# Performance work log

Measured on AMD Instinct MI355X. Metric: run time of the kernel, lower is better.

## Reference

```python
import jax, jax.numpy as jnp
import numpy as np

N = 50000      # n_nodes == ninput
E = 800000     # edges
NHID = 96
N_INTER = 6
EPS = 1e-12


def _l2norm(x):
    # F.normalize(x, p=2, dim=1) with eps=1e-12
    n = jnp.linalg.norm(x, axis=1, keepdims=True)
    return x / jnp.maximum(n, EPS)


def _sage(x, src, dst, Wl, bl, Wr, n):
    # PyG SAGEConv (mean aggr): lin_l(mean_{j in N(i)} x_j) + lin_r(x_i)
    agg = jax.ops.segment_sum(x[src], dst, num_segments=n)          # [N, nhid]
    deg = jax.ops.segment_sum(jnp.ones((src.shape[0],), x.dtype), dst, num_segments=n)
    agg = agg / jnp.maximum(deg, 1.0)[:, None]
    return agg @ Wl + bl + x @ Wr


def _mlp(x, W1, b1, W2, b2, W3, b3):
    # GNN-Bet score MLP (eval mode, dropout p=0): nhid -> 2*nhid -> 2*nhid -> 1
    h = jax.nn.relu(x @ W1 + b1)
    h = jax.nn.relu(h @ W2 + b2)
    return h @ W3 + b3


def setup_inputs() -> dict:
    key = jax.random.key(0)
    ks = jax.random.split(key, 16)
    s = 0.05
    inp = {
        'edge_index1': jax.random.randint(ks[0], (2, E), 0, N, dtype=jnp.int32),
        'edge_vals1': jax.random.uniform(ks[1], (E,), dtype=jnp.float32),
        'edge_index2': jax.random.randint(ks[2], (2, E), 0, N, dtype=jnp.int32),
        # GNN_Layer_Init: weight [ninput=N, nhid], bias [nhid]
        'gc1_W': jax.random.normal(ks[3], (N, NHID), dtype=jnp.float32) * s,
        'gc1_b': jnp.zeros((NHID,), jnp.float32),
        # 7 SAGEConv layers (6 intermediate + gc_last), stacked
        'sage_Wl': jax.random.normal(ks[4], (7, NHID, NHID), dtype=jnp.float32) * s,
        'sage_bl': jnp.zeros((7, NHID), jnp.float32),
        'sage_Wr': jax.random.normal(ks[5], (7, NHID, NHID), dtype=jnp.float32) * s,
        # score MLP
        'mlp_W1': jax.random.normal(ks[6], (NHID, 2 * NHID), dtype=jnp.float32) * s,
        'mlp_b1': jnp.zeros((2 * NHID,), jnp.float32),
        'mlp_W2': jax.random.normal(ks[7], (2 * NHID, 2 * NHID), dtype=jnp.float32) * s,
        'mlp_b2': jnp.zeros((2 * NHID,), jnp.float32),
        'mlp_W3': jax.random.normal(ks[8], (2 * NHID, 1), dtype=jnp.float32) * s,
        'mlp_b3': jnp.zeros((1,), jnp.float32),
    }
    return inp


def reference(edge_index1, edge_vals1, edge_index2, gc1_W, gc1_b,
              sage_Wl, sage_bl, sage_Wr,
              mlp_W1, mlp_b1, mlp_W2, mlp_b2, mlp_W3, mlp_b3):
    # gc1: spmm(adj1, W) -> out[i] = sum_j adj1[i,j] * W[j]
    dst1, src1 = edge_index1[0], edge_index1[1]
    h0 = jax.ops.segment_sum(gc1_W[src1] * edge_vals1[:, None], dst1, num_segments=N) + gc1_b
    x2_1 = _l2norm(jax.nn.relu(h0))

    src2, dst2 = edge_index2[0], edge_index2[1]

    # main trunk: 6 intermediate SAGE layers applied sequentially
    x = x2_1
    for i in range(N_INTER):
        x = _l2norm(jax.nn.relu(_sage(x, src2, dst2, sage_Wl[i], sage_bl[i], sage_Wr[i], N)))
    x_last = jax.nn.relu(_sage(x, src2, dst2, sage_Wl[N_INTER], sage_bl[N_INTER], sage_Wr[N_INTER], N))

    # scores: MLP on x2_1, on each intermediate layer applied once to x2_1, and on x_last
    score = _mlp(x2_1, mlp_W1, mlp_b1, mlp_W2, mlp_b2, mlp_W3, mlp_b3)
    for i in range(N_INTER):
        xi = _l2norm(jax.nn.relu(_sage(x2_1, src2, dst2, sage_Wl[i], sage_bl[i], sage_Wr[i], N)))
        score = score + _mlp(xi, mlp_W1, mlp_b1, mlp_W2, mlp_b2, mlp_W3, mlp_b3)
    score = score + _mlp(x_last, mlp_W1, mlp_b1, mlp_W2, mlp_b2, mlp_W3, mlp_b3)
    return score  # [N, 1]
```

## Files before the change

### kernel.cpp

```cpp
#include <hip/hip_runtime.h>

#define NH 96
#define NH2 192

typedef __attribute__((ext_vector_type(8))) short short8;
typedef __attribute__((ext_vector_type(4))) float f32x4;

__device__ __forceinline__ unsigned short f2b(float f) {
  unsigned u = __float_as_uint(f);
  unsigned r = (u + 0x7FFFu + ((u >> 16) & 1u)) >> 16;
  return (unsigned short)r;
}
__device__ __forceinline__ float blo(unsigned w) { return __uint_as_float(w << 16); }
__device__ __forceinline__ float bhi(unsigned w) { return __uint_as_float(w & 0xFFFF0000u); }
__device__ __forceinline__ float b2f(short v) { return __uint_as_float(((unsigned)(unsigned short)v) << 16); }

__device__ __forceinline__ unsigned cvt_pk(float lo, float hi) {
  unsigned r;
  asm("v_cvt_pk_bf16_f32 %0, %1, %2" : "=v"(r) : "v"(lo), "v"(hi));
  return r;
}

__device__ __forceinline__ short8 u4_to_s8(int a, int b, int c, int d) {
  union { int u[4]; short8 s; } x;
  x.u[0] = a; x.u[1] = b; x.u[2] = c; x.u[3] = d;
  return x.s;
}

#define MFMA(a, b, c) __builtin_amdgcn_mfma_f32_16x16x32_bf16((a), (b), (c), 0, 0, 0)
#define WFRAG(p, idx) (*(const short8*)((p) + ((idx) << 9) + (l << 3)))

__device__ __forceinline__ void stage(unsigned short* dst, const unsigned short* src, int nshorts,
                                      int tid, int nt) {
  const uint4* s = (const uint4*)src;
  uint4* d = (uint4*)dst;
  int nv = nshorts >> 3;
  for (int i = tid; i < nv; i += nt) d[i] = s[i];
}

__device__ __forceinline__ short8 xchg(unsigned p0lo, unsigned p0hi, unsigned p1lo, unsigned p1hi,
                                       int srcA, int srcB, int hi) {
  int a0 = __shfl((int)p0lo, srcA), a1 = __shfl((int)p0hi, srcA);
  int c0 = __shfl((int)p1lo, srcA), c1 = __shfl((int)p1hi, srcA);
  int b0 = __shfl((int)p0lo, srcB), b1 = __shfl((int)p0hi, srcB);
  int d0 = __shfl((int)p1lo, srcB), d1 = __shfl((int)p1hi, srcB);
  return u4_to_s8(hi ? c0 : a0, hi ? c1 : a1, hi ? d0 : b0, hi ? d1 : b1);
}


__global__ void k_count(const int* __restrict__ dst1, const int* __restrict__ dst2,
                        int* __restrict__ cnt1, int* __restrict__ cnt2, int E, int psize) {
  int p = blockIdx.x & 7;
  int e = (blockIdx.x >> 3) * blockDim.x + threadIdx.x;
  if (e >= E) return;
  int lo = p * psize, hi = lo + psize;
  int d = dst1[e];
  if (d >= lo && d < hi) atomicAdd(&cnt1[d], 1);
  int dd = dst2[e];
  if (dd >= lo && dd < hi) atomicAdd(&cnt2[dd], 1);
}


__global__ __launch_bounds__(256) void k_scanA(const int* __restrict__ cnt1, const int* __restrict__ cnt2,
                                               int* __restrict__ bs, int n) {
  int seg = blockIdx.y;
  const int* cnt = seg ? cnt2 : cnt1;
  int t = threadIdx.x;
  int idx = blockIdx.x * 1024 + t * 4;
  int sum = 0;
  if (idx + 3 < n) {
    int4 v = *(const int4*)(cnt + idx);
    sum = v.x + v.y + v.z + v.w;
  } else {
    for (int j = 0; j < 4; ++j) if (idx + j < n) sum += cnt[idx + j];
  }
  __shared__ int s[256];
  s[t] = sum;
  __syncthreads();
  for (int off = 128; off > 0; off >>= 1) {
    if (t < off) s[t] += s[t + off];
    __syncthreads();
  }
  if (t == 0) bs[seg * 64 + blockIdx.x] = s[0];
}

__global__ __launch_bounds__(128) void k_scanB(int* __restrict__ bs, int* __restrict__ rp1,
                                               int* __restrict__ rp2, int nb, int n) {
  int w = threadIdx.x >> 6, l = threadIdx.x & 63;
  int v = (l < nb) ? bs[w * 64 + l] : 0;
  int incl = v;
  for (int off = 1; off < 64; off <<= 1) {
    int u = __shfl_up(incl, off);
    if (l >= off) incl += u;
  }
  if (l < nb) bs[w * 64 + l] = incl - v;
  if (l == 63) {
    int* rp = w ? rp2 : rp1;
    rp[n] = incl;
  }
}

__global__ __launch_bounds__(256) void k_scanC(const int* __restrict__ cnt1, const int* __restrict__ cnt2,
                                               const int* __restrict__ bs,
                                               int* __restrict__ rp1, int* __restrict__ cur1,
                                               int* __restrict__ rp2, int* __restrict__ cur2, int n) {
  int seg = blockIdx.y;
  const int* cnt = seg ? cnt2 : cnt1;
  int* rp = seg ? rp2 : rp1;
  int* cur = seg ? cur2 : cur1;
  int t = threadIdx.x;
  int idx = blockIdx.x * 1024 + t * 4;
  int v[4] = {0, 0, 0, 0};
  if (idx + 3 < n) {
    int4 q = *(const int4*)(cnt + idx);
    v[0] = q.x; v[1] = q.y; v[2] = q.z; v[3] = q.w;
  } else {
    for (int j = 0; j < 4; ++j) if (idx + j < n) v[j] = cnt[idx + j];
  }
  int tsum = v[0] + v[1] + v[2] + v[3];
  __shared__ int s[256];
  s[t] = tsum;
  __syncthreads();
  for (int off = 1; off < 256; off <<= 1) {
    int u = (t >= off) ? s[t - off] : 0;
    __syncthreads();
    s[t] += u;
    __syncthreads();
  }
  int run = (t == 0 ? 0 : s[t - 1]) + bs[seg * 64 + blockIdx.x];
  for (int j = 0; j < 4; ++j) {
    if (idx + j < n) {
      rp[idx + j] = run;
      cur[idx + j] = run;
      run += v[j];
    }
  }
}

__global__ __launch_bounds__(1024) void k_scan(const int* __restrict__ cnt, int* __restrict__ rp,
                                               int* __restrict__ cur, int n) {
  __shared__ int s[1024];
  int tid = threadIdx.x;
  int chunk = (n + 1023) >> 10;
  int beg = tid * chunk;
  int end = min(beg + chunk, n);
  int sum = 0;
  for (int i = beg; i < end; ++i) sum += cnt[i];
  s[tid] = sum;
  __syncthreads();
  for (int off = 1; off < 1024; off <<= 1) {
    int v = (tid >= off) ? s[tid - off] : 0;
    __syncthreads();
    s[tid] += v;
    __syncthreads();
  }
  int excl = (tid == 0) ? 0 : s[tid - 1];
  for (int i = beg; i < end; ++i) { rp[i] = excl; cur[i] = excl; excl += cnt[i]; }
  if (tid == 1023) rp[n] = s[1023];
}

__global__ void k_scatter(const int* __restrict__ d1, const int* __restrict__ s1, const float* __restrict__ v1,
                          int* __restrict__ cur1, int2* __restrict__ c1sv,
                          const int* __restrict__ s2, const int* __restrict__ d2,
                          int* __restrict__ cur2, int* __restrict__ c2s, int E, int psize) {
  int p = blockIdx.x & 7;
  int e = (blockIdx.x >> 3) * blockDim.x + threadIdx.x;
  if (e >= E) return;
  int lo = p * psize, hi = lo + psize;
  int d = d1[e];
  if (d >= lo && d < hi) {
    int pos = atomicAdd(&cur1[d], 1);
    c1sv[pos] = make_int2(s1[e], __float_as_int(v1[e]));
  }
  int dd = d2[e];
  if (dd >= lo && dd < hi) {
    int pos = atomicAdd(&cur2[dd], 1);
    c2s[pos] = s2[e];
  }
}


__global__ void k_prep(const float* __restrict__ Wl, const float* __restrict__ Wr,
                       const float* __restrict__ W1, const float* __restrict__ W2,
                       const float* __restrict__ gW,
                       unsigned short* __restrict__ Wlp, unsigned short* __restrict__ Wrp,
                       unsigned short* __restrict__ W1p, unsigned short* __restrict__ W2p,
                       unsigned short* __restrict__ gwb, int gtotal) {
  int t = blockIdx.x * blockDim.x + threadIdx.x;
  if (t < 129024) {
    bool isR = t >= 64512;
    int u = isR ? t - 64512 : t;
    int i = u / 9216, v = u % 9216;
    int tt = v / 1536, r = v % 1536;
    int kf = r / 512, w = r % 512, l = w >> 3, j = w & 7;
    int c = l & 15, g = l >> 4;
    int k = kf * 32 + g * 8 + j, nn = tt * 16 + c;
    float val = (isR ? Wr : Wl)[i * 9216 + k * 96 + nn];
    (isR ? Wrp : Wlp)[u] = f2b(val);
  } else if (t < 147456) {
    int u = t - 129024;
    int tt = u / 1536, r = u % 1536;
    int kf = r / 512, w = r % 512, l = w >> 3, j = w & 7;
    int c = l & 15, g = l >> 4;
    int k = kf * 32 + g * 8 + j, nn = tt * 16 + c;
    W1p[u] = f2b(W1[k * 192 + nn]);
  } else if (t < 184320) {
    int u = t - 147456;
    int tt = u / 3072, r = u % 3072;
    int kf = r / 512, w = r % 512, l = w >> 3, j = w & 7;
    int c = l & 15, g = l >> 4;
    int k = kf * 32 + g * 8 + j, nn = tt * 16 + c;
    W2p[u] = f2b(W2[k * 192 + nn]);
  } else {
    int i = (t - 184320) * 4;
    if (i + 3 < gtotal) {
      float4 v = *(const float4*)(gW + i);
      ushort4 o;
      o.x = f2b(v.x); o.y = f2b(v.y); o.z = f2b(v.z); o.w = f2b(v.w);
      *(ushort4*)(gwb + i) = o;
    }
  }
}


__global__ __launch_bounds__(256) void k_gc1(const int* __restrict__ rp, const int2* __restrict__ cv,
                                             const unsigned short* __restrict__ Wb,
                                             const float* __restrict__ b, unsigned short* __restrict__ out, int n) {
  int gw = (blockIdx.x * 256 + threadIdx.x) >> 6;
  int l = threadIdx.x & 63;
  if (gw >= n) return;
  int s = rp[gw], e = rp[gw + 1];
  bool act = l < 48;
  float a0 = 0.f, a1 = 0.f, b0 = 0.f, b1 = 0.f, c0 = 0.f, c1 = 0.f, d0 = 0.f, d1 = 0.f;
  int i = s;
  for (; i + 3 < e; i += 4) {
    int2 q0 = cv[i], q1 = cv[i + 1], q2 = cv[i + 2], q3 = cv[i + 3];
    if (act) {
      unsigned w0 = *(const unsigned*)(Wb + (size_t)q0.x * NH + 2 * l);
      unsigned w1 = *(const unsigned*)(Wb + (size_t)q1.x * NH + 2 * l);
      unsigned w2 = *(const unsigned*)(Wb + (size_t)q2.x * NH + 2 * l);
      unsigned w3 = *(const unsigned*)(Wb + (size_t)q3.x * NH + 2 * l);
      float v0 = __int_as_float(q0.y), v1 = __int_as_float(q1.y);
      float v2 = __int_as_float(q2.y), v3 = __int_as_float(q3.y);
      a0 = fmaf(v0, blo(w0), a0); a1 = fmaf(v0, bhi(w0), a1);
      b0 = fmaf(v1, blo(w1), b0); b1 = fmaf(v1, bhi(w1), b1);
      c0 = fmaf(v2, blo(w2), c0); c1 = fmaf(v2, bhi(w2), c1);
      d0 = fmaf(v3, blo(w3), d0); d1 = fmaf(v3, bhi(w3), d1);
    }
  }
  for (; i < e; ++i) {
    int2 q0 = cv[i];
    if (act) {
      unsigned w0 = *(const unsigned*)(Wb + (size_t)q0.x * NH + 2 * l);
      float v0 = __int_as_float(q0.y);
      a0 = fmaf(v0, blo(w0), a0); a1 = fmaf(v0, bhi(w0), a1);
    }
  }
  a0 += b0 + c0 + d0; a1 += b1 + c1 + d1;
  if (act) {
    a0 = fmaxf(a0 + b[2 * l], 0.f);
    a1 = fmaxf(a1 + b[2 * l + 1], 0.f);
  } else { a0 = a1 = 0.f; }
  float ss = a0 * a0 + a1 * a1;
#pragma unroll
  for (int o = 1; o < 64; o <<= 1) ss += __shfl_xor(ss, o);
  float sc = 1.f / fmaxf(sqrtf(ss), 1e-12f);
  if (act) {
    unsigned pk = ((unsigned)f2b(a1 * sc) << 16) | f2b(a0 * sc);
    ((unsigned*)out)[(size_t)gw * 48 + l] = pk;
  }
}


__global__ __launch_bounds__(256) void k_agg(const int* __restrict__ rp, const int* __restrict__ csrc,
                                             const unsigned short* __restrict__ X,
                                             unsigned short* __restrict__ out, int n) {
  int gw = (blockIdx.x * 256 + threadIdx.x) >> 6;
  int l = threadIdx.x & 63;
  if (gw >= n) return;
  int s = rp[gw], e = rp[gw + 1];
  bool act = l < 48;
  float a0 = 0.f, a1 = 0.f, b0 = 0.f, b1 = 0.f, c0 = 0.f, c1 = 0.f, d0 = 0.f, d1 = 0.f;
  int i = s;
  for (; i + 3 < e; i += 4) {
    int s0 = csrc[i], s1 = csrc[i + 1], s2 = csrc[i + 2], s3 = csrc[i + 3];
    if (act) {
      unsigned w0 = *(const unsigned*)(X + (size_t)s0 * NH + 2 * l);
      unsigned w1 = *(const unsigned*)(X + (size_t)s1 * NH + 2 * l);
      unsigned w2 = *(const unsigned*)(X + (size_t)s2 * NH + 2 * l);
      unsigned w3 = *(const unsigned*)(X + (size_t)s3 * NH + 2 * l);
      a0 += blo(w0); a1 += bhi(w0);
      b0 += blo(w1); b1 += bhi(w1);
      c0 += blo(w2); c1 += bhi(w2);
      d0 += blo(w3); d1 += bhi(w3);
    }
  }
  for (; i < e; ++i) {
    int s0 = csrc[i];
    if (act) {
      unsigned w0 = *(const unsigned*)(X + (size_t)s0 * NH + 2 * l);
      a0 += blo(w0); a1 += bhi(w0);
    }
  }
  a0 += b0 + c0 + d0; a1 += b1 + c1 + d1;
  float inv = 1.f / fmaxf((float)(e - s), 1.f);
  if (act) {
    unsigned pk = ((unsigned)f2b(a1 * inv) << 16) | f2b(a0 * inv);
    ((unsigned*)out)[(size_t)gw * 48 + l] = pk;
  }
}


template <int EPI>
__global__ __launch_bounds__(256) void k_sageagg(const int* __restrict__ rp, const int* __restrict__ csrc,
                                                 const unsigned short* __restrict__ X,
                                                 const unsigned short* __restrict__ Wlp,
                                                 const unsigned short* __restrict__ Wrp,
                                                 const float* __restrict__ bias,
                                                 unsigned short* __restrict__ Y, int n) {
  __shared__ __align__(16) unsigned short sw[18432];
  int tid = threadIdx.x;
  int l = tid & 63;
  int m0 = (blockIdx.x * 4 + (tid >> 6)) * 16;
  int c = l & 15, g = l >> 4;

  stage(sw, Wlp, 9216, tid, 256);
  stage(sw + 9216, Wrp, 9216, tid, 256);
  __syncthreads();

  int nd = min(m0 + c, n - 1);
  int s = rp[nd], e = rp[nd + 1];

  float aa[3][8], bb[3][8];
#pragma unroll
  for (int kf = 0; kf < 3; ++kf)
#pragma unroll
    for (int j = 0; j < 8; ++j) { aa[kf][j] = 0.f; bb[kf][j] = 0.f; }

  const unsigned short* Xg = X + g * 8;
  int i = s;
  for (; i + 1 < e; i += 2) {
    const unsigned short* xr0 = Xg + (size_t)csrc[i] * NH;
    const unsigned short* xr1 = Xg + (size_t)csrc[i + 1] * NH;
    short8 a0 = *(const short8*)(xr0);
    short8 a1 = *(const short8*)(xr0 + 32);
    short8 a2 = *(const short8*)(xr0 + 64);
    short8 b0 = *(const short8*)(xr1);
    short8 b1 = *(const short8*)(xr1 + 32);
    short8 b2 = *(const short8*)(xr1 + 64);
#pragma unroll
    for (int j = 0; j < 8; ++j) {
      aa[0][j] += b2f(a0[j]); aa[1][j] += b2f(a1[j]); aa[2][j] += b2f(a2[j]);
      bb[0][j] += b2f(b0[j]); bb[1][j] += b2f(b1[j]); bb[2][j] += b2f(b2[j]);
    }
  }
  if (i < e) {
    const unsigned short* xr0 = Xg + (size_t)csrc[i] * NH;
    short8 a0 = *(const short8*)(xr0);
    short8 a1 = *(const short8*)(xr0 + 32);
    short8 a2 = *(const short8*)(xr0 + 64);
#pragma unroll
    for (int j = 0; j < 8; ++j) {
      aa[0][j] += b2f(a0[j]); aa[1][j] += b2f(a1[j]); aa[2][j] += b2f(a2[j]);
    }
  }
  float inv = 1.f / fmaxf((float)(e - s), 1.f);
  short8 af[3];
#pragma unroll
  for (int kf = 0; kf < 3; ++kf)
#pragma unroll
    for (int j = 0; j < 8; ++j) af[kf][j] = (short)f2b((aa[kf][j] + bb[kf][j]) * inv);

  size_t aoff = (size_t)nd * NH + g * 8;
  short8 xf[3];
#pragma unroll
  for (int kf = 0; kf < 3; ++kf) xf[kf] = *(const short8*)(X + aoff + kf * 32);

  f32x4 acc[6];
#pragma unroll
  for (int t = 0; t < 6; ++t) acc[t] = (f32x4){0.f, 0.f, 0.f, 0.f};
#pragma unroll
  for (int kf = 0; kf < 3; ++kf) {
#pragma unroll
    for (int t = 0; t < 6; ++t) {
      short8 wlf = WFRAG(sw, t * 3 + kf);
      acc[t] = MFMA(wlf, af[kf], acc[t]);
    }
#pragma unroll
    for (int t = 0; t < 6; ++t) {
      short8 wrf = WFRAG(sw + 9216, t * 3 + kf);
      acc[t] = MFMA(wrf, xf[kf], acc[t]);
    }
  }

  float v[6][4];
  float ss = 0.f;
#pragma unroll
  for (int t = 0; t < 6; ++t) {
    float4 bv = *(const float4*)(bias + t * 16 + g * 4);
#pragma unroll
    for (int r = 0; r < 4; ++r) {
      float x = fmaxf(acc[t][r] + ((const float*)&bv)[r], 0.f);
      v[t][r] = x;
      ss = fmaf(x, x, ss);
    }
  }
  if (EPI == 0) {
    ss += __shfl_xor(ss, 16);
    ss += __shfl_xor(ss, 32);
    float sc = 1.f / fmaxf(sqrtf(ss), 1e-12f);
#pragma unroll
    for (int t = 0; t < 6; ++t)
#pragma unroll
      for (int r = 0; r < 4; ++r) v[t][r] *= sc;
  }
  if (m0 + c < n) {
    unsigned short* yr = Y + (size_t)(m0 + c) * NH;
#pragma unroll
    for (int t = 0; t < 6; ++t)
      *(uint2*)(yr + t * 16 + g * 4) = make_uint2(cvt_pk(v[t][0], v[t][1]), cvt_pk(v[t][2], v[t][3]));
  }
}


__global__ __launch_bounds__(256) void k_mlp(const unsigned short* __restrict__ X,
                                             const unsigned short* __restrict__ W1p, const float* __restrict__ b1,
                                             const unsigned short* __restrict__ W2p, const float* __restrict__ b2,
                                             const float* __restrict__ W3, const float* __restrict__ b3,
                                             float* __restrict__ score, int n) {
  __shared__ __align__(16) unsigned short sw[18432];
  int tid = threadIdx.x;
  int l = tid & 63;
  int m0 = (blockIdx.x * 4 + (tid >> 6)) * 32;
  int c = l & 15, g = l >> 4;
  int srcA = c + ((g & 1) << 5), srcB = srcA + 16, hi = g >> 1;
  int rA = min(m0 + c, n - 1), rB = min(m0 + 16 + c, n - 1);

  stage(sw, W1p, 18432, tid, 256);

  short8 xf[2][3];
#pragma unroll
  for (int kf = 0; kf < 3; ++kf) {
    xf[0][kf] = *(const short8*)(X + (size_t)rA * NH + kf * 32 + g * 8);
    xf[1][kf] = *(const short8*)(X + (size_t)rB * NH + kf * 32 + g * 8);
  }
  __syncthreads();

  unsigned pk1[2][12][2];
#pragma unroll
  for (int t = 0; t < 12; ++t) {
    f32x4 a0 = (f32x4){0.f, 0.f, 0.f, 0.f};
    f32x4 a1 = (f32x4){0.f, 0.f, 0.f, 0.f};
#pragma unroll
    for (int kf = 0; kf < 3; ++kf) {
      short8 wf = WFRAG(sw, t * 3 + kf);
      a0 = MFMA(wf, xf[0][kf], a0);
      a1 = MFMA(wf, xf[1][kf], a1);
    }
    float4 bv = *(const float4*)(b1 + t * 16 + g * 4);
    pk1[0][t][0] = cvt_pk(fmaxf(a0[0] + bv.x, 0.f), fmaxf(a0[1] + bv.y, 0.f));
    pk1[0][t][1] = cvt_pk(fmaxf(a0[2] + bv.z, 0.f), fmaxf(a0[3] + bv.w, 0.f));
    pk1[1][t][0] = cvt_pk(fmaxf(a1[0] + bv.x, 0.f), fmaxf(a1[1] + bv.y, 0.f));
    pk1[1][t][1] = cvt_pk(fmaxf(a1[2] + bv.z, 0.f), fmaxf(a1[3] + bv.w, 0.f));
  }

  short8 af2[2][6];
#pragma unroll
  for (int kf = 0; kf < 6; ++kf) {
    af2[0][kf] = xchg(pk1[0][2 * kf][0], pk1[0][2 * kf][1], pk1[0][2 * kf + 1][0], pk1[0][2 * kf + 1][1], srcA, srcB, hi);
    af2[1][kf] = xchg(pk1[1][2 * kf][0], pk1[1][2 * kf][1], pk1[1][2 * kf + 1][0], pk1[1][2 * kf + 1][1], srcA, srcB, hi);
  }

  float sv0 = 0.f, sv1 = 0.f;
#pragma unroll
  for (int h = 0; h < 2; ++h) {
    __syncthreads();
    stage(sw, W2p + h * 18432, 18432, tid, 256);
    __syncthreads();
#pragma unroll
    for (int tt = 0; tt < 6; ++tt) {
      int t = h * 6 + tt;
      f32x4 a0 = (f32x4){0.f, 0.f, 0.f, 0.f};
      f32x4 a1 = (f32x4){0.f, 0.f, 0.f, 0.f};
#pragma unroll
      for (int kf = 0; kf < 6; ++kf) {
        short8 wf = WFRAG(sw, tt * 6 + kf);
        a0 = MFMA(wf, af2[0][kf], a0);
        a1 = MFMA(wf, af2[1][kf], a1);
      }
      float4 bv = *(const float4*)(b2 + t * 16 + g * 4);
      float4 wv3 = *(const float4*)(W3 + t * 16 + g * 4);
#pragma unroll
      for (int r = 0; r < 4; ++r) {
        sv0 = fmaf(fmaxf(a0[r] + ((const float*)&bv)[r], 0.f), ((const float*)&wv3)[r], sv0);
        sv1 = fmaf(fmaxf(a1[r] + ((const float*)&bv)[r], 0.f), ((const float*)&wv3)[r], sv1);
      }
    }
  }
  sv0 += __shfl_xor(sv0, 16); sv0 += __shfl_xor(sv0, 32);
  sv1 += __shfl_xor(sv1, 16); sv1 += __shfl_xor(sv1, 32);
  if (g == 0) {
    float b3v = b3[0];
    if (m0 + c < n) score[m0 + c] += sv0 + b3v;
    if (m0 + 16 + c < n) score[m0 + 16 + c] += sv1 + b3v;
  }
}


__global__ __launch_bounds__(512) void k_branch(const unsigned short* __restrict__ Ag,
                                                const unsigned short* __restrict__ X21,
                                                const unsigned short* __restrict__ Wlp,
                                                const unsigned short* __restrict__ Wrp,
                                                const float* __restrict__ sbl,
                                                const unsigned short* __restrict__ W1p, const float* __restrict__ b1,
                                                const unsigned short* __restrict__ W2p, const float* __restrict__ b2,
                                                const float* __restrict__ W3, const float* __restrict__ b3,
                                                unsigned short* __restrict__ Xb, float* __restrict__ score,
                                                int n, int nblk) {
  __shared__ __align__(16) unsigned short sw[18432];
  int bb = blockIdx.x / nblk;
  int blk = blockIdx.x - bb * nblk;
  int tid = threadIdx.x;
  int l = tid & 63;
  int m0 = (blk * 8 + (tid >> 6)) * 32;
  int c = l & 15, g = l >> 4;
  int srcA = c + ((g & 1) << 5), srcB = srcA + 16, hi = g >> 1;
  int rA = min(m0 + c, n - 1), rB = min(m0 + 16 + c, n - 1);
  size_t aoffA = (size_t)rA * NH + g * 8, aoffB = (size_t)rB * NH + g * 8;

  short8 af1[2][3];

  if (bb < 6) {
    const float* bl = sbl + (size_t)bb * NH;
    stage(sw, Wlp + (size_t)bb * 9216, 9216, tid, 512);
    stage(sw + 9216, Wrp + (size_t)bb * 9216, 9216, tid, 512);

    short8 agf[2][3], xf[2][3];
#pragma unroll
    for (int kf = 0; kf < 3; ++kf) {
      agf[0][kf] = *(const short8*)(Ag + aoffA + kf * 32);
      agf[1][kf] = *(const short8*)(Ag + aoffB + kf * 32);
      xf[0][kf] = *(const short8*)(X21 + aoffA + kf * 32);
      xf[1][kf] = *(const short8*)(X21 + aoffB + kf * 32);
    }
    __syncthreads();

    float v[2][6][4];
    float ss0 = 0.f, ss1 = 0.f;
#pragma unroll
    for (int t = 0; t < 6; ++t) {
      f32x4 a0 = (f32x4){0.f, 0.f, 0.f, 0.f};
      f32x4 a1 = (f32x4){0.f, 0.f, 0.f, 0.f};
#pragma unroll
      for (int kf = 0; kf < 3; ++kf) {
        short8 wlf = WFRAG(sw, t * 3 + kf);
        a0 = MFMA(wlf, agf[0][kf], a0);
        a1 = MFMA(wlf, agf[1][kf], a1);
        short8 wrf = WFRAG(sw + 9216, t * 3 + kf);
        a0 = MFMA(wrf, xf[0][kf], a0);
        a1 = MFMA(wrf, xf[1][kf], a1);
      }
      float4 bv = *(const float4*)(bl + t * 16 + g * 4);
#pragma unroll
      for (int r = 0; r < 4; ++r) {
        float x0 = fmaxf(a0[r] + ((const float*)&bv)[r], 0.f);
        float x1 = fmaxf(a1[r] + ((const float*)&bv)[r], 0.f);
        v[0][t][r] = x0; ss0 = fmaf(x0, x0, ss0);
        v[1][t][r] = x1; ss1 = fmaf(x1, x1, ss1);
      }
    }
    ss0 += __shfl_xor(ss0, 16); ss0 += __shfl_xor(ss0, 32);
    ss1 += __shfl_xor(ss1, 16); ss1 += __shfl_xor(ss1, 32);
    float sc0 = 1.f / fmaxf(sqrtf(ss0), 1e-12f);
    float sc1 = 1.f / fmaxf(sqrtf(ss1), 1e-12f);

    unsigned pk[2][6][2];
#pragma unroll
    for (int t = 0; t < 6; ++t) {
      pk[0][t][0] = cvt_pk(v[0][t][0] * sc0, v[0][t][1] * sc0);
      pk[0][t][1] = cvt_pk(v[0][t][2] * sc0, v[0][t][3] * sc0);
      pk[1][t][0] = cvt_pk(v[1][t][0] * sc1, v[1][t][1] * sc1);
      pk[1][t][1] = cvt_pk(v[1][t][2] * sc1, v[1][t][3] * sc1);
    }
    if (bb == 0) {
      if (m0 + c < n) {
        unsigned short* yr = Xb + (size_t)(m0 + c) * NH;
#pragma unroll
        for (int t = 0; t < 6; ++t) *(uint2*)(yr + t * 16 + g * 4) = make_uint2(pk[0][t][0], pk[0][t][1]);
      }
      if (m0 + 16 + c < n) {
        unsigned short* yr = Xb + (size_t)(m0 + 16 + c) * NH;
#pragma unroll
        for (int t = 0; t < 6; ++t) *(uint2*)(yr + t * 16 + g * 4) = make_uint2(pk[1][t][0], pk[1][t][1]);
      }
    }

    __syncthreads();
    stage(sw, W1p, 18432, tid, 512);
#pragma unroll
    for (int kf = 0; kf < 3; ++kf) {
      af1[0][kf] = xchg(pk[0][2 * kf][0], pk[0][2 * kf][1], pk[0][2 * kf + 1][0], pk[0][2 * kf + 1][1], srcA, srcB, hi);
      af1[1][kf] = xchg(pk[1][2 * kf][0], pk[1][2 * kf][1], pk[1][2 * kf + 1][0], pk[1][2 * kf + 1][1], srcA, srcB, hi);
    }
    __syncthreads();
  } else {
#pragma unroll
    for (int kf = 0; kf < 3; ++kf) {
      af1[0][kf] = *(const short8*)(X21 + aoffA + kf * 32);
      af1[1][kf] = *(const short8*)(X21 + aoffB + kf * 32);
    }
    stage(sw, W1p, 18432, tid, 512);
    __syncthreads();
  }

  unsigned pk1[2][12][2];
#pragma unroll
  for (int t = 0; t < 12; ++t) {
    f32x4 a0 = (f32x4){0.f, 0.f, 0.f, 0.f};
    f32x4 a1 = (f32x4){0.f, 0.f, 0.f, 0.f};
#pragma unroll
    for (int kf = 0; kf < 3; ++kf) {
      short8 wf = WFRAG(sw, t * 3 + kf);
      a0 = MFMA(wf, af1[0][kf], a0);
      a1 = MFMA(wf, af1[1][kf], a1);
    }
    float4 bv = *(const float4*)(b1 + t * 16 + g * 4);
    pk1[0][t][0] = cvt_pk(fmaxf(a0[0] + bv.x, 0.f), fmaxf(a0[1] + bv.y, 0.f));
    pk1[0][t][1] = cvt_pk(fmaxf(a0[2] + bv.z, 0.f), fmaxf(a0[3] + bv.w, 0.f));
    pk1[1][t][0] = cvt_pk(fmaxf(a1[0] + bv.x, 0.f), fmaxf(a1[1] + bv.y, 0.f));
    pk1[1][t][1] = cvt_pk(fmaxf(a1[2] + bv.z, 0.f), fmaxf(a1[3] + bv.w, 0.f));
  }

  short8 af2[2][6];
#pragma unroll
  for (int kf = 0; kf < 6; ++kf) {
    af2[0][kf] = xchg(pk1[0][2 * kf][0], pk1[0][2 * kf][1], pk1[0][2 * kf + 1][0], pk1[0][2 * kf + 1][1], srcA, srcB, hi);
    af2[1][kf] = xchg(pk1[1][2 * kf][0], pk1[1][2 * kf][1], pk1[1][2 * kf + 1][0], pk1[1][2 * kf + 1][1], srcA, srcB, hi);
  }
  float sv0 = 0.f, sv1 = 0.f;
#pragma unroll
  for (int h = 0; h < 2; ++h) {
    __syncthreads();
    stage(sw, W2p + h * 18432, 18432, tid, 512);
    __syncthreads();
#pragma unroll
    for (int tt = 0; tt < 6; ++tt) {
      int t = h * 6 + tt;
      f32x4 a0 = (f32x4){0.f, 0.f, 0.f, 0.f};
      f32x4 a1 = (f32x4){0.f, 0.f, 0.f, 0.f};
#pragma unroll
      for (int kf = 0; kf < 6; ++kf) {
        short8 wf = WFRAG(sw, tt * 6 + kf);
        a0 = MFMA(wf, af2[0][kf], a0);
        a1 = MFMA(wf, af2[1][kf], a1);
      }
      float4 bv = *(const float4*)(b2 + t * 16 + g * 4);
      float4 wv3 = *(const float4*)(W3 + t * 16 + g * 4);
#pragma unroll
      for (int r = 0; r < 4; ++r) {
        sv0 = fmaf(fmaxf(a0[r] + ((const float*)&bv)[r], 0.f), ((const float*)&wv3)[r], sv0);
        sv1 = fmaf(fmaxf(a1[r] + ((const float*)&bv)[r], 0.f), ((const float*)&wv3)[r], sv1);
      }
    }
  }
  sv0 += __shfl_xor(sv0, 16); sv0 += __shfl_xor(sv0, 32);
  sv1 += __shfl_xor(sv1, 16); sv1 += __shfl_xor(sv1, 32);
  if (g == 0) {
    float b3v = b3[0];
    if (m0 + c < n) atomicAdd(&score[m0 + c], sv0 + b3v);
    if (m0 + 16 + c < n) atomicAdd(&score[m0 + 16 + c], sv1 + b3v);
  }
}


extern "C" void kernel_launch(void* const* d_in, const int* in_sizes, int n_in,
                              void* d_out, int out_size, void* d_ws, size_t ws_size,
                              hipStream_t stream) {
  const int* ei1 = (const int*)d_in[0];
  const float* ev1 = (const float*)d_in[1];
  const int* ei2 = (const int*)d_in[2];
  const float* gW = (const float*)d_in[3];
  const float* gb = (const float*)d_in[4];
  const float* sWl = (const float*)d_in[5];
  const float* sbl = (const float*)d_in[6];
  const float* sWr = (const float*)d_in[7];
  const float* W1 = (const float*)d_in[8];
  const float* b1 = (const float*)d_in[9];
  const float* W2 = (const float*)d_in[10];
  const float* b2 = (const float*)d_in[11];
  const float* W3 = (const float*)d_in[12];
  const float* b3 = (const float*)d_in[13];
  float* score = (float*)d_out;

  const int E = in_sizes[0] / 2;
  const int n = in_sizes[3] / NH;

  const int* d1 = ei1;
  const int* s1 = ei1 + E;
  const int* s2 = ei2;
  const int* d2 = ei2 + E;

  char* w = (char*)d_ws;
  auto alloc = [&](size_t bytes) {
    char* p = w;
    w += (bytes + 255) & ~(size_t)255;
    return p;
  };
  int* cnt1 = (int*)alloc((size_t)n * 4);
  int* cnt2 = (int*)alloc((size_t)n * 4);
  int* cur1 = (int*)alloc((size_t)n * 4);
  int* cur2 = (int*)alloc((size_t)n * 4);
  int* rp1 = (int*)alloc((size_t)(n + 1) * 4);
  int* rp2 = (int*)alloc((size_t)(n + 1) * 4);
  int* bs = (int*)alloc(128 * 4);
  int2* c1sv = (int2*)alloc((size_t)E * 8);
  int* c2s = (int*)alloc((size_t)E * 4);
  unsigned short* gwb = (unsigned short*)alloc((size_t)n * NH * 2);
  unsigned short* wlp = (unsigned short*)alloc((size_t)7 * NH * NH * 2);
  unsigned short* wrp = (unsigned short*)alloc((size_t)7 * NH * NH * 2);
  unsigned short* w1p = (unsigned short*)alloc((size_t)NH * NH2 * 2);
  unsigned short* w2p = (unsigned short*)alloc((size_t)NH2 * NH2 * 2);
  unsigned short* x21 = (unsigned short*)alloc((size_t)n * NH * 2);
  unsigned short* Ag = (unsigned short*)alloc((size_t)n * NH * 2);
  unsigned short* xb = (unsigned short*)alloc((size_t)n * NH * 2);
  unsigned short* tb = (unsigned short*)alloc((size_t)n * NH * 2);

  size_t zbytes = (size_t)((char*)cur1 - (char*)cnt1) + (size_t)n * 4;
  hipMemsetAsync(cnt1, 0, zbytes, stream);
  hipMemsetAsync(score, 0, (size_t)n * 4, stream);

  int eb = (E + 255) / 256;
  int nb4 = (n + 3) / 4;
  int sblk = (n + 63) / 64;
  int gblk = (n + 127) / 128;
  int nblk = (n + 255) / 256;
  int psize = (n + 7) / 8;
  int nb1024 = (n + 1023) / 1024;
  int gtotal = n * NH;
  int prep_threads = 184320 + gtotal / 4;

  k_count<<<eb * 8, 256, 0, stream>>>(d1, d2, cnt1, cnt2, E, psize);
  if (nb1024 <= 64) {
    k_scanA<<<dim3(nb1024, 2), 256, 0, stream>>>(cnt1, cnt2, bs, n);
    k_scanB<<<1, 128, 0, stream>>>(bs, rp1, rp2, nb1024, n);
    k_scanC<<<dim3(nb1024, 2), 256, 0, stream>>>(cnt1, cnt2, bs, rp1, cur1, rp2, cur2, n);
  } else {
    k_scan<<<1, 1024, 0, stream>>>(cnt1, rp1, cur1, n);
    k_scan<<<1, 1024, 0, stream>>>(cnt2, rp2, cur2, n);
  }
  k_scatter<<<eb * 8, 256, 0, stream>>>(d1, s1, ev1, cur1, c1sv, s2, d2, cur2, c2s, E, psize);

  k_prep<<<(prep_threads + 255) / 256, 256, 0, stream>>>(sWl, sWr, W1, W2, gW,
                                                         wlp, wrp, w1p, w2p, gwb, gtotal);

  k_gc1<<<nb4, 256, 0, stream>>>(rp1, c1sv, gwb, gb, x21, n);

  k_agg<<<nb4, 256, 0, stream>>>(rp2, c2s, x21, Ag, n);

  k_branch<<<7 * nblk, 512, 0, stream>>>(Ag, x21, wlp, wrp, sbl, w1p, b1, w2p, b2, W3, b3,
                                         xb, score, n, nblk);

  unsigned short* xc = xb;
  unsigned short* xn = tb;
  for (int i = 1; i < 6; ++i) {
    k_sageagg<0><<<sblk, 256, 0, stream>>>(rp2, c2s, xc, wlp + (size_t)i * 9216,
                                           wrp + (size_t)i * 9216, sbl + (size_t)i * NH, xn, n);
    unsigned short* tmp = xc; xc = xn; xn = tmp;
  }

  k_sageagg<1><<<sblk, 256, 0, stream>>>(rp2, c2s, xc, wlp + (size_t)6 * 9216,
                                         wrp + (size_t)6 * 9216, sbl + (size_t)6 * NH, xn, n);
  k_mlp<<<gblk, 256, 0, stream>>>(xn, w1p, b1, w2p, b2, W3, b3, score, n);

  (void)n_in; (void)out_size; (void)ws_size;
}
```

Before: 553.4 us.

## Merge weight prep into count kernel and overlap branch MLPs with trunk layer

Weight/bf16 prep is merged into the edge-count kernel as extra blocks, so both run in one launch. The seven-branch kernel is split: branch 0 and branch 6 (which produces the trunk input) run first. A mega kernel then runs branches 1-5 alongside the first trunk SAGE layer, using 8-wave blocks for the trunk part. This removes launches and fills the GPU during the small sequential trunk layer, at the cost of more complex block dispatch and mixed workloads sharing a launch.

```diff
diff --git a/kernel.cpp b/kernel.cpp
--- a/kernel.cpp
+++ b/kernel.cpp
@@ -49,144 +49,25 @@
 
 
 __global__ void k_count(const int* __restrict__ dst1, const int* __restrict__ dst2,
-                        int* __restrict__ cnt1, int* __restrict__ cnt2, int E, int psize) {
-  int p = blockIdx.x & 7;
-  int e = (blockIdx.x >> 3) * blockDim.x + threadIdx.x;
-  if (e >= E) return;
-  int lo = p * psize, hi = lo + psize;
-  int d = dst1[e];
-  if (d >= lo && d < hi) atomicAdd(&cnt1[d], 1);
-  int dd = dst2[e];
-  if (dd >= lo && dd < hi) atomicAdd(&cnt2[dd], 1);
-}
-
-
-__global__ __launch_bounds__(256) void k_scanA(const int* __restrict__ cnt1, const int* __restrict__ cnt2,
-                                               int* __restrict__ bs, int n) {
-  int seg = blockIdx.y;
-  const int* cnt = seg ? cnt2 : cnt1;
-  int t = threadIdx.x;
-  int idx = blockIdx.x * 1024 + t * 4;
-  int sum = 0;
-  if (idx + 3 < n) {
-    int4 v = *(const int4*)(cnt + idx);
-    sum = v.x + v.y + v.z + v.w;
-  } else {
-    for (int j = 0; j < 4; ++j) if (idx + j < n) sum += cnt[idx + j];
-  }
-  __shared__ int s[256];
-  s[t] = sum;
-  __syncthreads();
-  for (int off = 128; off > 0; off >>= 1) {
-    if (t < off) s[t] += s[t + off];
-    __syncthreads();
-  }
-  if (t == 0) bs[seg * 64 + blockIdx.x] = s[0];
-}
-
-__global__ __launch_bounds__(128) void k_scanB(int* __restrict__ bs, int* __restrict__ rp1,
-                                               int* __restrict__ rp2, int nb, int n) {
-  int w = threadIdx.x >> 6, l = threadIdx.x & 63;
-  int v = (l < nb) ? bs[w * 64 + l] : 0;
-  int incl = v;
-  for (int off = 1; off < 64; off <<= 1) {
-    int u = __shfl_up(incl, off);
-    if (l >= off) incl += u;
-  }
-  if (l < nb) bs[w * 64 + l] = incl - v;
-  if (l == 63) {
-    int* rp = w ? rp2 : rp1;
-    rp[n] = incl;
-  }
-}
-
-__global__ __launch_bounds__(256) void k_scanC(const int* __restrict__ cnt1, const int* __restrict__ cnt2,
-                                               const int* __restrict__ bs,
-                                               int* __restrict__ rp1, int* __restrict__ cur1,
-                                               int* __restrict__ rp2, int* __restrict__ cur2, int n) {
-  int seg = blockIdx.y;
-  const int* cnt = seg ? cnt2 : cnt1;
-  int* rp = seg ? rp2 : rp1;
-  int* cur = seg ? cur2 : cur1;
-  int t = threadIdx.x;
-  int idx = blockIdx.x * 1024 + t * 4;
-  int v[4] = {0, 0, 0, 0};
-  if (idx + 3 < n) {
-    int4 q = *(const int4*)(cnt + idx);
-    v[0] = q.x; v[1] = q.y; v[2] = q.z; v[3] = q.w;
-  } else {
-    for (int j = 0; j < 4; ++j) if (idx + j < n) v[j] = cnt[idx + j];
-  }
-  int tsum = v[0] + v[1] + v[2] + v[3];
-  __shared__ int s[256];
-  s[t] = tsum;
-  __syncthreads();
-  for (int off = 1; off < 256; off <<= 1) {
-    int u = (t >= off) ? s[t - off] : 0;
-    __syncthreads();
-    s[t] += u;
-    __syncthreads();
-  }
-  int run = (t == 0 ? 0 : s[t - 1]) + bs[seg * 64 + blockIdx.x];
-  for (int j = 0; j < 4; ++j) {
-    if (idx + j < n) {
-      rp[idx + j] = run;
-      cur[idx + j] = run;
-      run += v[j];
-    }
-  }
-}
-
-__global__ __launch_bounds__(1024) void k_scan(const int* __restrict__ cnt, int* __restrict__ rp,
-                                               int* __restrict__ cur, int n) {
-  __shared__ int s[1024];
-  int tid = threadIdx.x;
-  int chunk = (n + 1023) >> 10;
-  int beg = tid * chunk;
-  int end = min(beg + chunk, n);
-  int sum = 0;
-  for (int i = beg; i < end; ++i) sum += cnt[i];
-  s[tid] = sum;
-  __syncthreads();
-  for (int off = 1; off < 1024; off <<= 1) {
-    int v = (tid >= off) ? s[tid - off] : 0;
-    __syncthreads();
-    s[tid] += v;
-    __syncthreads();
-  }
-  int excl = (tid == 0) ? 0 : s[tid - 1];
-  for (int i = beg; i < end; ++i) { rp[i] = excl; cur[i] = excl; excl += cnt[i]; }
-  if (tid == 1023) rp[n] = s[1023];
-}
-
-__global__ void k_scatter(const int* __restrict__ d1, const int* __restrict__ s1, const float* __restrict__ v1,
-                          int* __restrict__ cur1, int2* __restrict__ c1sv,
-                          const int* __restrict__ s2, const int* __restrict__ d2,
-                          int* __restrict__ cur2, int* __restrict__ c2s, int E, int psize) {
-  int p = blockIdx.x & 7;
-  int e = (blockIdx.x >> 3) * blockDim.x + threadIdx.x;
-  if (e >= E) return;
-  int lo = p * psize, hi = lo + psize;
-  int d = d1[e];
-  if (d >= lo && d < hi) {
-    int pos = atomicAdd(&cur1[d], 1);
-    c1sv[pos] = make_int2(s1[e], __float_as_int(v1[e]));
-  }
-  int dd = d2[e];
-  if (dd >= lo && dd < hi) {
-    int pos = atomicAdd(&cur2[dd], 1);
-    c2s[pos] = s2[e];
-  }
-}
-
-
-__global__ void k_prep(const float* __restrict__ Wl, const float* __restrict__ Wr,
-                       const float* __restrict__ W1, const float* __restrict__ W2,
-                       const float* __restrict__ gW,
-                       unsigned short* __restrict__ Wlp, unsigned short* __restrict__ Wrp,
-                       unsigned short* __restrict__ W1p, unsigned short* __restrict__ W2p,
-                       unsigned short* __restrict__ gwb, int gtotal) {
-  int t = blockIdx.x * blockDim.x + threadIdx.x;
+                        int* __restrict__ cnt1, int* __restrict__ cnt2, int E, int psize, int cblocks,
+                        const float* __restrict__ Wl, const float* __restrict__ Wr,
+                        const float* __restrict__ W1, const float* __restrict__ W2,
+                        const float* __restrict__ gW,
+                        unsigned short* __restrict__ Wlp, unsigned short* __restrict__ Wrp,
+                        unsigned short* __restrict__ W1p, unsigned short* __restrict__ W2p,
+                        unsigned short* __restrict__ gwb, int gtotal) {
+  if (blockIdx.x < (unsigned)cblocks) {
+    int p = blockIdx.x & 7;
+    int e = (blockIdx.x >> 3) * blockDim.x + threadIdx.x;
+    if (e >= E) return;
+    int lo = p * psize, hi = lo + psize;
+    int d = dst1[e];
+    if (d >= lo && d < hi) atomicAdd(&cnt1[d], 1);
+    int dd = dst2[e];
+    if (dd >= lo && dd < hi) atomicAdd(&cnt2[dd], 1);
+    return;
+  }
+  int t = (blockIdx.x - cblocks) * blockDim.x + threadIdx.x;
   if (t < 129024) {
     bool isR = t >= 64512;
     int u = isR ? t - 64512 : t;
@@ -223,6 +104,125 @@
 }
 
 
+__global__ __launch_bounds__(256) void k_scanA(const int* __restrict__ cnt1, const int* __restrict__ cnt2,
+                                               int* __restrict__ bs, int n) {
+  int seg = blockIdx.y;
+  const int* cnt = seg ? cnt2 : cnt1;
+  int t = threadIdx.x;
+  int idx = blockIdx.x * 1024 + t * 4;
+  int sum = 0;
+  if (idx + 3 < n) {
+    int4 v = *(const int4*)(cnt + idx);
+    sum = v.x + v.y + v.z + v.w;
+  } else {
+    for (int j = 0; j < 4; ++j) if (idx + j < n) sum += cnt[idx + j];
+  }
+  __shared__ int s[256];
+  s[t] = sum;
+  __syncthreads();
+  for (int off = 128; off > 0; off >>= 1) {
+    if (t < off) s[t] += s[t + off];
+    __syncthreads();
+  }
+  if (t == 0) bs[seg * 64 + blockIdx.x] = s[0];
+}
+
+__global__ __launch_bounds__(128) void k_scanB(int* __restrict__ bs, int* __restrict__ rp1,
+                                               int* __restrict__ rp2, int nb, int n) {
+  int w = threadIdx.x >> 6, l = threadIdx.x & 63;
+  int v = (l < nb) ? bs[w * 64 + l] : 0;
+  int incl = v;
+  for (int off = 1; off < 64; off <<= 1) {
+    int u = __shfl_up(incl, off);
+    if (l >= off) incl += u;
+  }
+  if (l < nb) bs[w * 64 + l] = incl - v;
+  if (l == 63) {
+    int* rp = w ? rp2 : rp1;
+    rp[n] = incl;
+  }
+}
+
+__global__ __launch_bounds__(256) void k_scanC(const int* __restrict__ cnt1, const int* __restrict__ cnt2,
+                                               const int* __restrict__ bs,
+                                               int* __restrict__ rp1, int* __restrict__ cur1,
+                                               int* __restrict__ rp2, int* __restrict__ cur2, int n) {
+  int seg = blockIdx.y;
+  const int* cnt = seg ? cnt2 : cnt1;
+  int* rp = seg ? rp2 : rp1;
+  int* cur = seg ? cur2 : cur1;
+  int t = threadIdx.x;
+  int idx = blockIdx.x * 1024 + t * 4;
+  int v[4] = {0, 0, 0, 0};
+  if (idx + 3 < n) {
+    int4 q = *(const int4*)(cnt + idx);
+    v[0] = q.x; v[1] = q.y; v[2] = q.z; v[3] = q.w;
+  } else {
+    for (int j = 0; j < 4; ++j) if (idx + j < n) v[j] = cnt[idx + j];
+  }
+  int tsum = v[0] + v[1] + v[2] + v[3];
+  __shared__ int s[256];
+  s[t] = tsum;
+  __syncthreads();
+  for (int off = 1; off < 256; off <<= 1) {
+    int u = (t >= off) ? s[t - off] : 0;
+    __syncthreads();
+    s[t] += u;
+    __syncthreads();
+  }
+  int run = (t == 0 ? 0 : s[t - 1]) + bs[seg * 64 + blockIdx.x];
+  for (int j = 0; j < 4; ++j) {
+    if (idx + j < n) {
+      rp[idx + j] = run;
+      cur[idx + j] = run;
+      run += v[j];
+    }
+  }
+}
+
+__global__ __launch_bounds__(1024) void k_scan(const int* __restrict__ cnt, int* __restrict__ rp,
+                                               int* __restrict__ cur, int n) {
+  __shared__ int s[1024];
+  int tid = threadIdx.x;
+  int chunk = (n + 1023) >> 10;
+  int beg = tid * chunk;
+  int end = min(beg + chunk, n);
+  int sum = 0;
+  for (int i = beg; i < end; ++i) sum += cnt[i];
+  s[tid] = sum;
+  __syncthreads();
+  for (int off = 1; off < 1024; off <<= 1) {
+    int v = (tid >= off) ? s[tid - off] : 0;
+    __syncthreads();
+    s[tid] += v;
+    __syncthreads();
+  }
+  int excl = (tid == 0) ? 0 : s[tid - 1];
+  for (int i = beg; i < end; ++i) { rp[i] = excl; cur[i] = excl; excl += cnt[i]; }
+  if (tid == 1023) rp[n] = s[1023];
+}
+
+__global__ void k_scatter(const int* __restrict__ d1, const int* __restrict__ s1, const float* __restrict__ v1,
+                          int* __restrict__ cur1, int2* __restrict__ c1sv,
+                          const int* __restrict__ s2, const int* __restrict__ d2,
+                          int* __restrict__ cur2, int* __restrict__ c2s, int E, int psize) {
+  int p = blockIdx.x & 7;
+  int e = (blockIdx.x >> 3) * blockDim.x + threadIdx.x;
+  if (e >= E) return;
+  int lo = p * psize, hi = lo + psize;
+  int d = d1[e];
+  if (d >= lo && d < hi) {
+    int pos = atomicAdd(&cur1[d], 1);
+    c1sv[pos] = make_int2(s1[e], __float_as_int(v1[e]));
+  }
+  int dd = d2[e];
+  if (dd >= lo && dd < hi) {
+    int pos = atomicAdd(&cur2[dd], 1);
+    c2s[pos] = s2[e];
+  }
+}
+
+
 __global__ __launch_bounds__(256) void k_gc1(const int* __restrict__ rp, const int2* __restrict__ cv,
                                              const unsigned short* __restrict__ Wb,
                                              const float* __restrict__ b, unsigned short* __restrict__ out, int n) {
@@ -312,20 +312,20 @@
 
 
 template <int EPI>
-__global__ __launch_bounds__(256) void k_sageagg(const int* __restrict__ rp, const int* __restrict__ csrc,
-                                                 const unsigned short* __restrict__ X,
-                                                 const unsigned short* __restrict__ Wlp,
-                                                 const unsigned short* __restrict__ Wrp,
-                                                 const float* __restrict__ bias,
-                                                 unsigned short* __restrict__ Y, int n) {
-  __shared__ __align__(16) unsigned short sw[18432];
+__device__ __forceinline__ void sage_body(int blk, int nwaves, unsigned short* sw,
+                                          const int* __restrict__ rp, const int* __restrict__ csrc,
+                                          const unsigned short* __restrict__ X,
+                                          const unsigned short* __restrict__ Wlp,
+                                          const unsigned short* __restrict__ Wrp,
+                                          const float* __restrict__ bias,
+                                          unsigned short* __restrict__ Y, int n) {
   int tid = threadIdx.x;
   int l = tid & 63;
-  int m0 = (blockIdx.x * 4 + (tid >> 6)) * 16;
+  int m0 = (blk * nwaves + (tid >> 6)) * 16;
   int c = l & 15, g = l >> 4;
 
-  stage(sw, Wlp, 9216, tid, 256);
-  stage(sw + 9216, Wrp, 9216, tid, 256);
+  stage(sw, Wlp, 9216, tid, nwaves * 64);
+  stage(sw + 9216, Wrp, 9216, tid, nwaves * 64);
   __syncthreads();
 
   int nd = min(m0 + c, n - 1);
@@ -420,6 +420,17 @@
     for (int t = 0; t < 6; ++t)
       *(uint2*)(yr + t * 16 + g * 4) = make_uint2(cvt_pk(v[t][0], v[t][1]), cvt_pk(v[t][2], v[t][3]));
   }
+}
+
+template <int EPI>
+__global__ __launch_bounds__(256) void k_sageagg(const int* __restrict__ rp, const int* __restrict__ csrc,
+                                                 const unsigned short* __restrict__ X,
+                                                 const unsigned short* __restrict__ Wlp,
+                                                 const unsigned short* __restrict__ Wrp,
+                                                 const float* __restrict__ bias,
+                                                 unsigned short* __restrict__ Y, int n) {
+  __shared__ __align__(16) unsigned short sw[18432];
+  sage_body<EPI>(blockIdx.x, 4, sw, rp, csrc, X, Wlp, Wrp, bias, Y, n);
 }
 
 
@@ -507,19 +518,16 @@
 }
 
 
-__global__ __launch_bounds__(512) void k_branch(const unsigned short* __restrict__ Ag,
-                                                const unsigned short* __restrict__ X21,
-                                                const unsigned short* __restrict__ Wlp,
-                                                const unsigned short* __restrict__ Wrp,
-                                                const float* __restrict__ sbl,
-                                                const unsigned short* __restrict__ W1p, const float* __restrict__ b1,
-                                                const unsigned short* __restrict__ W2p, const float* __restrict__ b2,
-                                                const float* __restrict__ W3, const float* __restrict__ b3,
-                                                unsigned short* __restrict__ Xb, float* __restrict__ score,
-                                                int n, int nblk) {
-  __shared__ __align__(16) unsigned short sw[18432];
-  int bb = blockIdx.x / nblk;
-  int blk = blockIdx.x - bb * nblk;
+__device__ __forceinline__ void branch_body(int bb, int blk, unsigned short* sw,
+                                            const unsigned short* __restrict__ Ag,
+                                            const unsigned short* __restrict__ X21,
+                                            const unsigned short* __restrict__ Wlp,
+                                            const unsigned short* __restrict__ Wrp,
+                                            const float* __restrict__ sbl,
+                                            const unsigned short* __restrict__ W1p, const float* __restrict__ b1,
+                                            const unsigned short* __restrict__ W2p, const float* __restrict__ b2,
+                                            const float* __restrict__ W3, const float* __restrict__ b3,
+                                            unsigned short* __restrict__ Xb, float* __restrict__ score, int n) {
   int tid = threadIdx.x;
   int l = tid & 63;
   int m0 = (blk * 8 + (tid >> 6)) * 32;
@@ -669,6 +677,45 @@
     float b3v = b3[0];
     if (m0 + c < n) atomicAdd(&score[m0 + c], sv0 + b3v);
     if (m0 + 16 + c < n) atomicAdd(&score[m0 + 16 + c], sv1 + b3v);
+  }
+}
+
+__global__ __launch_bounds__(512) void k_branchA(const unsigned short* __restrict__ Ag,
+                                                 const unsigned short* __restrict__ X21,
+                                                 const unsigned short* __restrict__ Wlp,
+                                                 const unsigned short* __restrict__ Wrp,
+                                                 const float* __restrict__ sbl,
+                                                 const unsigned short* __restrict__ W1p, const float* __restrict__ b1,
+                                                 const unsigned short* __restrict__ W2p, const float* __restrict__ b2,
+                                                 const float* __restrict__ W3, const float* __restrict__ b3,
+                                                 unsigned short* __restrict__ Xb, float* __restrict__ score,
+                                                 int n, int nblk) {
+  __shared__ __align__(16) unsigned short sw[18432];
+  int bb = (blockIdx.x >= (unsigned)nblk) ? 6 : 0;
+  int blk = blockIdx.x - (bb ? nblk : 0);
+  branch_body(bb, blk, sw, Ag, X21, Wlp, Wrp, sbl, W1p, b1, W2p, b2, W3, b3, Xb, score, n);
+}
+
+__global__ __launch_bounds__(512) void k_mega(const unsigned short* __restrict__ Ag,
+                                              const unsigned short* __restrict__ X21,
+                                              const unsigned short* __restrict__ Wlp,
+                                              const unsigned short* __restrict__ Wrp,
+                                              const float* __restrict__ sbl,
+                                              const unsigned short* __restrict__ W1p, const float* __restrict__ b1,
+                                              const unsigned short* __restrict__ W2p, const float* __restrict__ b2,
+                                              const float* __restrict__ W3, const float* __restrict__ b3,
+                                              float* __restrict__ score,
+                                              const int* __restrict__ rp2, const int* __restrict__ c2s,
+                                              const unsigned short* __restrict__ Xb, unsigned short* __restrict__ Tb,
+                                              int n, int nblk, int nbranch) {
+  __shared__ __align__(16) unsigned short sw[18432];
+  if (blockIdx.x < (unsigned)nbranch) {
+    int bb = 1 + blockIdx.x / nblk;
+    int blk = blockIdx.x - (bb - 1) * nblk;
+    branch_body(bb, blk, sw, Ag, X21, Wlp, Wrp, sbl, W1p, b1, W2p, b2, W3, b3, nullptr, score, n);
+  } else {
+    sage_body<0>(blockIdx.x - nbranch, 8, sw, rp2, c2s, Xb,
+                 Wlp + 9216, Wrp + 9216, sbl + NH, Tb, n);
   }
 }
 
@@ -734,12 +781,14 @@
   int sblk = (n + 63) / 64;
   int gblk = (n + 127) / 128;
   int nblk = (n + 255) / 256;
+  int tblk8 = (n + 127) / 128;
   int psize = (n + 7) / 8;
   int nb1024 = (n + 1023) / 1024;
   int gtotal = n * NH;
-  int prep_threads = 184320 + gtotal / 4;
-
-  k_count<<<eb * 8, 256, 0, stream>>>(d1, d2, cnt1, cnt2, E, psize);
+  int prep_blocks = (184320 + gtotal / 4 + 255) / 256;
+
+  k_count<<<eb * 8 + prep_blocks, 256, 0, stream>>>(d1, d2, cnt1, cnt2, E, psize, eb * 8,
+                                                    sWl, sWr, W1, W2, gW, wlp, wrp, w1p, w2p, gwb, gtotal);
   if (nb1024 <= 64) {
     k_scanA<<<dim3(nb1024, 2), 256, 0, stream>>>(cnt1, cnt2, bs, n);
     k_scanB<<<1, 128, 0, stream>>>(bs, rp1, rp2, nb1024, n);
@@ -750,19 +799,19 @@
   }
   k_scatter<<<eb * 8, 256, 0, stream>>>(d1, s1, ev1, cur1, c1sv, s2, d2, cur2, c2s, E, psize);
 
-  k_prep<<<(prep_threads + 255) / 256, 256, 0, stream>>>(sWl, sWr, W1, W2, gW,
-                                                         wlp, wrp, w1p, w2p, gwb, gtotal);
-
   k_gc1<<<nb4, 256, 0, stream>>>(rp1, c1sv, gwb, gb, x21, n);
 
   k_agg<<<nb4, 256, 0, stream>>>(rp2, c2s, x21, Ag, n);
 
-  k_branch<<<7 * nblk, 512, 0, stream>>>(Ag, x21, wlp, wrp, sbl, w1p, b1, w2p, b2, W3, b3,
-                                         xb, score, n, nblk);
-
-  unsigned short* xc = xb;
-  unsigned short* xn = tb;
-  for (int i = 1; i < 6; ++i) {
+  k_branchA<<<2 * nblk, 512, 0, stream>>>(Ag, x21, wlp, wrp, sbl, w1p, b1, w2p, b2, W3, b3,
+                                          xb, score, n, nblk);
+
+  k_mega<<<5 * nblk + tblk8, 512, 0, stream>>>(Ag, x21, wlp, wrp, sbl, w1p, b1, w2p, b2, W3, b3,
+                                               score, rp2, c2s, xb, tb, n, nblk, 5 * nblk);
+
+  unsigned short* xc = tb;
+  unsigned short* xn = xb;
+  for (int i = 2; i < 6; ++i) {
     k_sageagg<0><<<sblk, 256, 0, stream>>>(rp2, c2s, xc, wlp + (size_t)i * 9216,
                                            wrp + (size_t)i * 9216, sbl + (size_t)i * NH, xn, n);
     unsigned short* tmp = xc; xc = xn; xn = tmp;
```

Result: no change. 554.1 us (+0.1%).
